# Kernel tuning notes

Measured on AMD Instinct MI355X. Metric: run time of the kernel, lower is better.

Reference implementation:

```python
import jax, jax.numpy as jnp
import numpy as np

S = 128  # sqrt_n; feature dim n = S*S = 16384


def _perm(x, s):
    # rearrange '... (m n) -> ... (n m)' with m = n = s: transpose the s x s
    # factorization of the last dim.
    return jnp.swapaxes(x.reshape(*x.shape[:-1], s, s), -1, -2).reshape(x.shape)


def _bdmm(x, w):
    # blockdiag_matmul: view last dim as (blocks=s, m=s), per-block GEMM.
    b, m = w.shape[0], w.shape[-1]
    xv = x.reshape(*x.shape[:-1], b, m)
    return jnp.einsum('bnm,...bm->...bn', w, xv).reshape(x.shape)


def setup_inputs() -> dict:
    key = jax.random.key(0)
    k1, k2, k3, k4 = jax.random.split(key, 4)
    n = S * S
    scale = jnp.float32(1.0 / np.sqrt(S))
    return {
        'x': jax.random.normal(k1, (2, 2048, n), dtype=jnp.float32),
        'L': jax.random.normal(k2, (S, S, S), dtype=jnp.float32) * scale,
        'R': jax.random.normal(k3, (S, S, S), dtype=jnp.float32) * scale,
        'bias': jax.random.normal(k4, (n,), dtype=jnp.float32) * jnp.float32(0.02),
    }


def reference(x, L, R, bias):
    s = L.shape[0]
    x = _perm(x, s)
    x = _bdmm(x, L)
    x = _perm(x, s)
    x = _bdmm(x, R)
    x = _perm(x, s)
    return x + bias
```

## Files before the change

### kernel.cpp

```cpp
#include <hip/hip_runtime.h>

typedef __bf16 bf16x8 __attribute__((ext_vector_type(8)));
typedef float  f32x4  __attribute__((ext_vector_type(4)));

static __device__ __forceinline__ unsigned short f32_to_bf16(float f) {
  union { float f; unsigned u; } v; v.f = f;
  unsigned r = v.u + 0x7fffu + ((v.u >> 16) & 1u);
  return (unsigned short)(r >> 16);
}
static __device__ __forceinline__ float bf16_to_f32(unsigned short h) {
  union { unsigned u; float f; } v; v.u = ((unsigned)h) << 16;
  return v.f;
}

__global__ __launch_bounds__(256) void k_cvt(const float* __restrict__ src,
                                             unsigned short* __restrict__ dst, int n4) {
  int i = blockIdx.x * 256 + threadIdx.x;
  if (i >= n4) return;
  float4 v = ((const float4*)src)[i];
  uint2 o;
  o.x = (unsigned)f32_to_bf16(v.x) | ((unsigned)f32_to_bf16(v.y) << 16);
  o.y = (unsigned)f32_to_bf16(v.z) | ((unsigned)f32_to_bf16(v.w) << 16);
  ((uint2*)dst)[i] = o;
}

__global__ __launch_bounds__(256) void k_t1(const float* __restrict__ x,
                                            unsigned short* __restrict__ xP) {
  __shared__ unsigned short Ts[64 * 72];
  const int c0 = blockIdx.x * 64;
  const int r0 = blockIdx.y * 64;
  const int tid = threadIdx.x;
#pragma unroll
  for (int it = 0; it < 4; ++it) {
    int flat = it * 256 + tid;
    int rl = flat >> 4, cs = flat & 15;
    float4 v = ((const float4*)(x + (size_t)(r0 + rl) * 16384 + c0))[cs];
    Ts[(cs * 4 + 0) * 72 + rl] = f32_to_bf16(v.x);
    Ts[(cs * 4 + 1) * 72 + rl] = f32_to_bf16(v.y);
    Ts[(cs * 4 + 2) * 72 + rl] = f32_to_bf16(v.z);
    Ts[(cs * 4 + 3) * 72 + rl] = f32_to_bf16(v.w);
  }
  __syncthreads();
#pragma unroll
  for (int it = 0; it < 2; ++it) {
    int flat = it * 256 + tid;
    int cl = flat >> 3, rs = flat & 7;
    int c = c0 + cl;
    int orow = ((c & 127) << 7) | (c >> 7);
    uint4 v = *(const uint4*)&Ts[cl * 72 + rs * 8];
    ((uint4*)(xP + (size_t)orow * 4096 + r0))[rs] = v;
  }
}

__global__ __launch_bounds__(256) void k_bgemm(const unsigned short* __restrict__ Wb,
                                               const unsigned short* __restrict__ In,
                                               unsigned short* __restrict__ Out) {
  __shared__ unsigned short As[128 * 128];
  __shared__ unsigned short Bt[128 * 128];
  const int b  = blockIdx.y;
  const int r0 = blockIdx.x * 128;
  const int tid = threadIdx.x;

  {
    const uint4* g = (const uint4*)(Wb + (size_t)b * 16384);
#pragma unroll
    for (int it = 0; it < 8; ++it) {
      int flat = it * 256 + tid;
      int row = flat >> 4, ks = flat & 15;
      uint4 v = g[flat];
      *(uint4*)&As[row * 128 + ((ks ^ (row & 15)) << 3)] = v;
    }
  }
  {
    int kb = tid >> 4;
    int rs = tid & 15;
    uint4 v[8];
#pragma unroll
    for (int kk = 0; kk < 8; ++kk)
      v[kk] = ((const uint4*)(In + (size_t)(b * 128 + kb * 8 + kk) * 4096 + r0))[rs];
    const unsigned short* s = (const unsigned short*)v;
#pragma unroll
    for (int rr = 0; rr < 8; ++rr) {
      unsigned short o[8];
#pragma unroll
      for (int kk = 0; kk < 8; ++kk) o[kk] = s[kk * 8 + rr];
      int row = rs * 8 + rr;
      *(uint4*)&Bt[row * 128 + ((kb ^ (row & 15)) << 3)] = *(const uint4*)o;
    }
  }
  __syncthreads();

  const int wave = tid >> 6, lane = tid & 63;
  const int q = lane >> 4, l16 = lane & 15;
  const int wm = (wave >> 1) * 64, wn = (wave & 1) * 64;
  f32x4 acc[4][4] = {};

#pragma unroll
  for (int ks = 0; ks < 4; ++ks) {
    bf16x8 af[4], bfr[4];
#pragma unroll
    for (int f = 0; f < 4; ++f) {
      int arow = wm + f * 16 + l16;
      af[f]  = *(const bf16x8*)&As[arow * 128 + (((ks * 4 + q) ^ (arow & 15)) << 3)];
      int brow = wn + f * 16 + l16;
      bfr[f] = *(const bf16x8*)&Bt[brow * 128 + (((ks * 4 + q) ^ (brow & 15)) << 3)];
    }
#pragma unroll
    for (int fi = 0; fi < 4; ++fi)
#pragma unroll
      for (int fj = 0; fj < 4; ++fj)
        acc[fi][fj] = __builtin_amdgcn_mfma_f32_16x16x32_bf16(af[fi], bfr[fj], acc[fi][fj], 0, 0, 0);
  }

#pragma unroll
  for (int fi = 0; fi < 4; ++fi) {
#pragma unroll
    for (int fj = 0; fj < 4; ++fj) {
      int col = r0 + wn + fj * 16 + l16;
#pragma unroll
      for (int p = 0; p < 4; ++p) {
        int row = wm + fi * 16 + q * 4 + p;
        Out[(size_t)(row * 128 + b) * 4096 + col] = f32_to_bf16(acc[fi][fj][p]);
      }
    }
  }
}

__global__ __launch_bounds__(256) void k_t2(const unsigned short* __restrict__ OP,
                                            const float* __restrict__ bias,
                                            float* __restrict__ out) {
  __shared__ float Ts[64 * 68];
  const int c0 = blockIdx.x * 64;
  const int r0 = blockIdx.y * 64;
  const int tid = threadIdx.x;
#pragma unroll
  for (int it = 0; it < 2; ++it) {
    int flat = it * 256 + tid;
    int cl = flat >> 3, rs = flat & 7;
    uint4 v = ((const uint4*)(OP + (size_t)(c0 + cl) * 4096 + r0))[rs];
    float bc = bias[c0 + cl];
    const unsigned short* s = (const unsigned short*)&v;
#pragma unroll
    for (int e = 0; e < 8; ++e)
      Ts[(rs * 8 + e) * 68 + cl] = bf16_to_f32(s[e]) + bc;
  }
  __syncthreads();
#pragma unroll
  for (int it = 0; it < 4; ++it) {
    int flat = it * 256 + tid;
    int rl = flat >> 4, cs = flat & 15;
    float4 v = *(const float4*)&Ts[rl * 68 + cs * 4];
    ((float4*)(out + (size_t)(r0 + rl) * 16384 + c0))[cs] = v;
  }
}

extern "C" void kernel_launch(void* const* d_in, const int* in_sizes, int n_in,
                              void* d_out, int out_size, void* d_ws, size_t ws_size,
                              hipStream_t stream) {
  const float* x    = (const float*)d_in[0];
  const float* L    = (const float*)d_in[1];
  const float* R    = (const float*)d_in[2];
  const float* bias = (const float*)d_in[3];
  float* out = (float*)d_out;

  const size_t SZ_W  = (size_t)4 << 20;
  const size_t SZ_XP = (size_t)128 << 20;
  if (ws_size < 2 * SZ_W + 2 * SZ_XP) return;

  char* ws = (char*)d_ws;
  unsigned short* Lb = (unsigned short*)ws;
  unsigned short* Rb = (unsigned short*)(ws + SZ_W);
  unsigned short* xP = (unsigned short*)(ws + 2 * SZ_W);
  unsigned short* TP = (unsigned short*)(ws + 2 * SZ_W + SZ_XP);
  unsigned short* OP = xP;

  k_cvt<<<2048, 256, 0, stream>>>(L, Lb, 524288);
  k_cvt<<<2048, 256, 0, stream>>>(R, Rb, 524288);
  k_t1<<<dim3(256, 64), 256, 0, stream>>>(x, xP);
  k_bgemm<<<dim3(32, 128), 256, 0, stream>>>(Lb, xP, TP);
  k_bgemm<<<dim3(32, 128), 256, 0, stream>>>(Rb, TP, OP);
  k_t2<<<dim3(256, 64), 256, 0, stream>>>(OP, bias, out);
}
```

Measured before the change: 635.6 us.

## Fuse transposes into batched GEMM stages, reducing pipeline to three kernels

Replaces the transpose, two block-diagonal GEMMs and final transpose kernels with two fused stages. Stage A reads fp32 x directly, converts it to bf16 into LDS and multiplies by L, writing an intermediate in a layout chosen for stage B. Stage B multiplies by R and adds bias directly into the fp32 output. The two weight conversions are merged into one launch. This removes two full-size intermediate round-trips through HBM, at the cost of weight fragments now being read straight from global memory inside the MFMA loop rather than staged in LDS.

```diff
diff --git a/kernel.cpp b/kernel.cpp
--- a/kernel.cpp
+++ b/kernel.cpp
@@ -8,149 +8,162 @@
   unsigned r = v.u + 0x7fffu + ((v.u >> 16) & 1u);
   return (unsigned short)(r >> 16);
 }
-static __device__ __forceinline__ float bf16_to_f32(unsigned short h) {
-  union { unsigned u; float f; } v; v.u = ((unsigned)h) << 16;
-  return v.f;
-}
 
-__global__ __launch_bounds__(256) void k_cvt(const float* __restrict__ src,
-                                             unsigned short* __restrict__ dst, int n4) {
+__global__ __launch_bounds__(256) void k_cvt2(const float* __restrict__ L,
+                                              const float* __restrict__ R,
+                                              unsigned short* __restrict__ Lb,
+                                              unsigned short* __restrict__ Rb) {
   int i = blockIdx.x * 256 + threadIdx.x;
-  if (i >= n4) return;
-  float4 v = ((const float4*)src)[i];
+  const float* s; unsigned short* d; int idx;
+  if (i < 524288) { s = L; d = Lb; idx = i; } else { s = R; d = Rb; idx = i - 524288; }
+  float4 v = ((const float4*)s)[idx];
   uint2 o;
   o.x = (unsigned)f32_to_bf16(v.x) | ((unsigned)f32_to_bf16(v.y) << 16);
   o.y = (unsigned)f32_to_bf16(v.z) | ((unsigned)f32_to_bf16(v.w) << 16);
-  ((uint2*)dst)[i] = o;
+  ((uint2*)d)[idx] = o;
 }
 
-__global__ __launch_bounds__(256) void k_t1(const float* __restrict__ x,
-                                            unsigned short* __restrict__ xP) {
-  __shared__ unsigned short Ts[64 * 72];
-  const int c0 = blockIdx.x * 64;
-  const int r0 = blockIdx.y * 64;
+__global__ __launch_bounds__(256, 2) void k_stageA(const float* __restrict__ x,
+                                                   const unsigned short* __restrict__ Lb,
+                                                   unsigned short* __restrict__ T) {
+  __shared__ unsigned short Xs[16 * 16 * 128];
+  const int bid = blockIdx.x;
+  const int u = bid & 7, h = (bid >> 3) & 1, t = (bid >> 4) & 31, P = bid >> 9;
+  const int r0 = ((t << 3) + u) << 4;
+  const int m0 = ((P << 1) + h) << 4;
   const int tid = threadIdx.x;
-#pragma unroll
-  for (int it = 0; it < 4; ++it) {
-    int flat = it * 256 + tid;
-    int rl = flat >> 4, cs = flat & 15;
-    float4 v = ((const float4*)(x + (size_t)(r0 + rl) * 16384 + c0))[cs];
-    Ts[(cs * 4 + 0) * 72 + rl] = f32_to_bf16(v.x);
-    Ts[(cs * 4 + 1) * 72 + rl] = f32_to_bf16(v.y);
-    Ts[(cs * 4 + 2) * 72 + rl] = f32_to_bf16(v.z);
-    Ts[(cs * 4 + 3) * 72 + rl] = f32_to_bf16(v.w);
-  }
-  __syncthreads();
-#pragma unroll
-  for (int it = 0; it < 2; ++it) {
-    int flat = it * 256 + tid;
-    int cl = flat >> 3, rs = flat & 7;
-    int c = c0 + cl;
-    int orow = ((c & 127) << 7) | (c >> 7);
-    uint4 v = *(const uint4*)&Ts[cl * 72 + rs * 8];
-    ((uint4*)(xP + (size_t)orow * 4096 + r0))[rs] = v;
-  }
-}
-
-__global__ __launch_bounds__(256) void k_bgemm(const unsigned short* __restrict__ Wb,
-                                               const unsigned short* __restrict__ In,
-                                               unsigned short* __restrict__ Out) {
-  __shared__ unsigned short As[128 * 128];
-  __shared__ unsigned short Bt[128 * 128];
-  const int b  = blockIdx.y;
-  const int r0 = blockIdx.x * 128;
-  const int tid = threadIdx.x;
+  const int w = tid >> 6, lane = tid & 63;
 
   {
-    const uint4* g = (const uint4*)(Wb + (size_t)b * 16384);
+    const int mg = tid & 3, kg = (tid >> 2) & 15;
 #pragma unroll
-    for (int it = 0; it < 8; ++it) {
-      int flat = it * 256 + tid;
-      int row = flat >> 4, ks = flat & 15;
-      uint4 v = g[flat];
-      *(uint4*)&As[row * 128 + ((ks ^ (row & 15)) << 3)] = v;
-    }
-  }
-  {
-    int kb = tid >> 4;
-    int rs = tid & 15;
-    uint4 v[8];
+    for (int it = 0; it < 4; ++it) {
+      const int r = (it << 2) + w;
+      const float* g = x + (size_t)(r0 + r) * 16384 + m0 + (mg << 2);
+      float4 v[8];
 #pragma unroll
-    for (int kk = 0; kk < 8; ++kk)
-      v[kk] = ((const uint4*)(In + (size_t)(b * 128 + kb * 8 + kk) * 4096 + r0))[rs];
-    const unsigned short* s = (const unsigned short*)v;
+      for (int kk = 0; kk < 8; ++kk) v[kk] = *(const float4*)(g + (((kg << 3) + kk) << 7));
+      const int cw = (kg ^ r) << 3;
 #pragma unroll
-    for (int rr = 0; rr < 8; ++rr) {
-      unsigned short o[8];
+      for (int mm = 0; mm < 4; ++mm) {
+        unsigned short o[8];
 #pragma unroll
-      for (int kk = 0; kk < 8; ++kk) o[kk] = s[kk * 8 + rr];
-      int row = rs * 8 + rr;
-      *(uint4*)&Bt[row * 128 + ((kb ^ (row & 15)) << 3)] = *(const uint4*)o;
+        for (int kk = 0; kk < 8; ++kk) o[kk] = f32_to_bf16(((const float*)&v[kk])[mm]);
+        *(uint4*)&Xs[((((mg << 2) + mm) << 4) + r) * 128 + cw] = *(const uint4*)o;
+      }
     }
   }
   __syncthreads();
 
-  const int wave = tid >> 6, lane = tid & 63;
-  const int q = lane >> 4, l16 = lane & 15;
-  const int wm = (wave >> 1) * 64, wn = (wave & 1) * 64;
-  f32x4 acc[4][4] = {};
+  const int mh = w & 1, jh = w >> 1;
+  const int l16 = lane & 15, q = lane >> 4;
+  const unsigned short* Lw = Lb + (size_t)(m0 + (mh << 3)) * 16384 + (q << 3);
 
 #pragma unroll
-  for (int ks = 0; ks < 4; ++ks) {
-    bf16x8 af[4], bfr[4];
+  for (int phase = 0; phase < 2; ++phase) {
+    const int jb = (phase << 6) + (jh << 5);
+    f32x4 acc[8][2] = {};
 #pragma unroll
-    for (int f = 0; f < 4; ++f) {
-      int arow = wm + f * 16 + l16;
-      af[f]  = *(const bf16x8*)&As[arow * 128 + (((ks * 4 + q) ^ (arow & 15)) << 3)];
-      int brow = wn + f * 16 + l16;
-      bfr[f] = *(const bf16x8*)&Bt[brow * 128 + (((ks * 4 + q) ^ (brow & 15)) << 3)];
+    for (int ks = 0; ks < 4; ++ks) {
+      bf16x8 Af[2][8];
+#pragma unroll
+      for (int jf = 0; jf < 2; ++jf)
+#pragma unroll
+        for (int mm = 0; mm < 8; ++mm)
+          Af[jf][mm] = *(const bf16x8*)(Lw + (size_t)mm * 16384
+                                        + ((jb + (jf << 4) + l16) << 7) + (ks << 5));
+      bf16x8 Bf[8];
+#pragma unroll
+      for (int mm = 0; mm < 8; ++mm)
+        Bf[mm] = *(const bf16x8*)&Xs[((((mh << 3) + mm) << 4) + l16) * 128
+                                     + ((((ks << 2) + q) ^ l16) << 3)];
+#pragma unroll
+      for (int jf = 0; jf < 2; ++jf)
+#pragma unroll
+        for (int mm = 0; mm < 8; ++mm)
+          acc[mm][jf] = __builtin_amdgcn_mfma_f32_16x16x32_bf16(Af[jf][mm], Bf[mm],
+                                                                acc[mm][jf], 0, 0, 0);
     }
 #pragma unroll
-    for (int fi = 0; fi < 4; ++fi)
-#pragma unroll
-      for (int fj = 0; fj < 4; ++fj)
-        acc[fi][fj] = __builtin_amdgcn_mfma_f32_16x16x32_bf16(af[fi], bfr[fj], acc[fi][fj], 0, 0, 0);
-  }
-
-#pragma unroll
-  for (int fi = 0; fi < 4; ++fi) {
-#pragma unroll
-    for (int fj = 0; fj < 4; ++fj) {
-      int col = r0 + wn + fj * 16 + l16;
+    for (int jf = 0; jf < 2; ++jf)
 #pragma unroll
       for (int p = 0; p < 4; ++p) {
-        int row = wm + fi * 16 + q * 4 + p;
-        Out[(size_t)(row * 128 + b) * 4096 + col] = f32_to_bf16(acc[fi][fj][p]);
+        const int j = jb + (jf << 4) + (q << 2) + p;
+        unsigned short o[8];
+#pragma unroll
+        for (int mm = 0; mm < 8; ++mm) o[mm] = f32_to_bf16(acc[mm][jf][p]);
+        *(uint4*)(T + ((size_t)j * 4096 + r0 + l16) * 128 + m0 + (mh << 3)) = *(const uint4*)o;
       }
-    }
   }
 }
 
-__global__ __launch_bounds__(256) void k_t2(const unsigned short* __restrict__ OP,
-                                            const float* __restrict__ bias,
-                                            float* __restrict__ out) {
-  __shared__ float Ts[64 * 68];
-  const int c0 = blockIdx.x * 64;
-  const int r0 = blockIdx.y * 64;
+__global__ __launch_bounds__(256, 2) void k_stageB(const unsigned short* __restrict__ T,
+                                                   const unsigned short* __restrict__ Rb,
+                                                   const float* __restrict__ bias,
+                                                   float* __restrict__ out) {
+  __shared__ unsigned short Ts[16 * 16 * 128];
+  const int r0 = blockIdx.x << 4;
+  const int j0 = blockIdx.y << 4;
   const int tid = threadIdx.x;
+  const int w = tid >> 6, lane = tid & 63;
+
+  {
+    const int seg = tid & 15, r = tid >> 4;
+    const int cw = (seg ^ r) << 3;
 #pragma unroll
-  for (int it = 0; it < 2; ++it) {
-    int flat = it * 256 + tid;
-    int cl = flat >> 3, rs = flat & 7;
-    uint4 v = ((const uint4*)(OP + (size_t)(c0 + cl) * 4096 + r0))[rs];
-    float bc = bias[c0 + cl];
-    const unsigned short* s = (const unsigned short*)&v;
-#pragma unroll
-    for (int e = 0; e < 8; ++e)
-      Ts[(rs * 8 + e) * 68 + cl] = bf16_to_f32(s[e]) + bc;
+    for (int jl = 0; jl < 16; ++jl) {
+      uint4 v = *(const uint4*)(T + ((size_t)(j0 + jl) * 4096 + r0 + r) * 128 + (seg << 3));
+      *(uint4*)&Ts[((jl << 4) + r) * 128 + cw] = v;
+    }
   }
   __syncthreads();
+
+  const int jh = w & 1, ih = w >> 1;
+  const int l16 = lane & 15, q = lane >> 4;
+  const unsigned short* Rw = Rb + (size_t)(j0 + (jh << 3)) * 16384 + (l16 << 7) + (q << 3);
+
 #pragma unroll
-  for (int it = 0; it < 4; ++it) {
-    int flat = it * 256 + tid;
-    int rl = flat >> 4, cs = flat & 15;
-    float4 v = *(const float4*)&Ts[rl * 68 + cs * 4];
-    ((float4*)(out + (size_t)(r0 + rl) * 16384 + c0))[cs] = v;
+  for (int phase = 0; phase < 2; ++phase) {
+    const int ib = (phase << 6) + (ih << 5);
+    f32x4 acc[8][2] = {};
+#pragma unroll
+    for (int ms = 0; ms < 4; ++ms) {
+      bf16x8 Af[2][8];
+#pragma unroll
+      for (int ifr = 0; ifr < 2; ++ifr)
+#pragma unroll
+        for (int jj = 0; jj < 8; ++jj)
+          Af[ifr][jj] = *(const bf16x8*)(Rw + (size_t)jj * 16384
+                                         + ((ib + (ifr << 4)) << 7) + (ms << 5));
+      bf16x8 Bf[8];
+#pragma unroll
+      for (int jj = 0; jj < 8; ++jj)
+        Bf[jj] = *(const bf16x8*)&Ts[((((jh << 3) + jj) << 4) + l16) * 128
+                                     + ((((ms << 2) + q) ^ l16) << 3)];
+#pragma unroll
+      for (int ifr = 0; ifr < 2; ++ifr)
+#pragma unroll
+        for (int jj = 0; jj < 8; ++jj)
+          acc[jj][ifr] = __builtin_amdgcn_mfma_f32_16x16x32_bf16(Af[ifr][jj], Bf[jj],
+                                                                 acc[jj][ifr], 0, 0, 0);
+    }
+#pragma unroll
+    for (int ifr = 0; ifr < 2; ++ifr)
+#pragma unroll
+      for (int p = 0; p < 4; ++p) {
+        const int i = ib + (ifr << 4) + (q << 2) + p;
+        const size_t fb = (size_t)i * 128 + j0 + (jh << 3);
+        const float4 b0 = *(const float4*)(bias + fb);
+        const float4 b1 = *(const float4*)(bias + fb + 4);
+        float4 o0, o1;
+        o0.x = acc[0][ifr][p] + b0.x; o0.y = acc[1][ifr][p] + b0.y;
+        o0.z = acc[2][ifr][p] + b0.z; o0.w = acc[3][ifr][p] + b0.w;
+        o1.x = acc[4][ifr][p] + b1.x; o1.y = acc[5][ifr][p] + b1.y;
+        o1.z = acc[6][ifr][p] + b1.z; o1.w = acc[7][ifr][p] + b1.w;
+        float* op = out + (size_t)(r0 + l16) * 16384 + fb;
+        *(float4*)op = o0;
+        *(float4*)(op + 4) = o1;
+      }
   }
 }
 
@@ -163,21 +176,16 @@
   const float* bias = (const float*)d_in[3];
   float* out = (float*)d_out;
 
-  const size_t SZ_W  = (size_t)4 << 20;
-  const size_t SZ_XP = (size_t)128 << 20;
-  if (ws_size < 2 * SZ_W + 2 * SZ_XP) return;
+  const size_t SZ_W = (size_t)4 << 20;
+  const size_t SZ_T = (size_t)128 << 20;
+  if (ws_size < 2 * SZ_W + SZ_T) return;
 
   char* ws = (char*)d_ws;
   unsigned short* Lb = (unsigned short*)ws;
   unsigned short* Rb = (unsigned short*)(ws + SZ_W);
-  unsigned short* xP = (unsigned short*)(ws + 2 * SZ_W);
-  unsigned short* TP = (unsigned short*)(ws + 2 * SZ_W + SZ_XP);
-  unsigned short* OP = xP;
+  unsigned short* Tw = (unsigned short*)(ws + 2 * SZ_W);
 
-  k_cvt<<<2048, 256, 0, stream>>>(L, Lb, 524288);
-  k_cvt<<<2048, 256, 0, stream>>>(R, Rb, 524288);
-  k_t1<<<dim3(256, 64), 256, 0, stream>>>(x, xP);
-  k_bgemm<<<dim3(32, 128), 256, 0, stream>>>(Lb, xP, TP);
-  k_bgemm<<<dim3(32, 128), 256, 0, stream>>>(Rb, TP, OP);
-  k_t2<<<dim3(256, 64), 256, 0, stream>>>(OP, bias, out);
+  k_cvt2<<<4096, 256, 0, stream>>>(L, R, Lb, Rb);
+  k_stageA<<<2048, 256, 0, stream>>>(x, Lb, Tw);
+  k_stageB<<<dim3(256, 8), 256, 0, stream>>>(Tw, Rb, bias, out);
 }
```

New measurement: 874.8 us. +37.6%, slower.
